# Optimization experiments

Measured on AMD Instinct MI355X. Metric: run time of the kernel, lower is better.

## Reference

```python
import jax, jax.numpy as jnp
import numpy as np

B, S, F, H = 2, 2048, 1024, 16
D = F // H  # 64 head dim


def setup_inputs() -> dict:
    key = jax.random.key(0)
    ks = jax.random.split(key, 11)
    std = 1.0 / np.sqrt(F)
    inp = {
        "q": jax.random.normal(ks[0], (B, S, F), dtype=jnp.float32),
        "k": jax.random.normal(ks[1], (B, S, F), dtype=jnp.float32),
        "v": jax.random.normal(ks[2], (B, S, F), dtype=jnp.float32),
        "wq_w": jax.random.normal(ks[3], (F, F), dtype=jnp.float32) * std,
        "wq_b": jnp.zeros((F,), dtype=jnp.float32),
        "wk_w": jax.random.normal(ks[4], (F, F), dtype=jnp.float32) * std,
        "wk_b": jnp.zeros((F,), dtype=jnp.float32),
        "wv_w": jax.random.normal(ks[5], (F, F), dtype=jnp.float32) * std,
        "wv_b": jnp.zeros((F,), dtype=jnp.float32),
        "fc_w": jax.random.normal(ks[6], (F, F), dtype=jnp.float32) * std,
        "fc_b": jnp.zeros((F,), dtype=jnp.float32),
    }
    return inp


def _split_heads(x):
    # [B, S, F] -> [B, H, S, D]
    return x.reshape(B, S, H, D).transpose(0, 2, 1, 3)


def reference(q, k, v, wq_w, wq_b, wk_w, wk_b, wv_w, wv_b, fc_w, fc_b):
    # Linear projections (torch Linear: x @ W^T + b)
    qh = _split_heads(q @ wq_w.T + wq_b)
    kh = _split_heads(k @ wk_w.T + wk_b)
    vh = _split_heads(v @ wv_w.T + wv_b)
    # scaled dot product attention, explicit [B,H,S,S] scores as in source
    scale = 1.0 / np.sqrt(D)
    scores = jnp.einsum("bhqd,bhkd->bhqk", qh, kh) * scale
    attn = jax.nn.softmax(scores, axis=-1)
    ctx = jnp.einsum("bhqk,bhkd->bhqd", attn, vh)
    # merge heads: [B,H,S,D] -> [B,S,F]
    concat = ctx.transpose(0, 2, 1, 3).reshape(B, S, F)
    out = concat @ fc_w.T + fc_b
    out = jax.nn.relu(out)  # activation=F.relu_ default
    return (out, attn)
```

## Files before the change

### kernel.cpp

```cpp
#include <hip/hip_runtime.h>
#include <stdint.h>

#define DEV __device__ __forceinline__

using f32x4  = __attribute__((ext_vector_type(4))) float;
using bf16x8 = __attribute__((ext_vector_type(8))) __bf16;
using bf16x4 = __attribute__((ext_vector_type(4))) __bf16;

static constexpr int SEQ  = 2048;
static constexpr int FEA  = 1024;
static constexpr int NHEAD = 16;
static constexpr int MROWS = 4096;
static constexpr float QK_SCALE = 0.18033688011112042f;

DEV f32x4 mfma16(bf16x8 a, bf16x8 b, f32x4 c) {
  return __builtin_amdgcn_mfma_f32_16x16x32_bf16(a, b, c, 0, 0, 0);
}

DEV void gload16(const void* g, void* l) {
  __builtin_amdgcn_global_load_lds((__attribute__((address_space(1))) void*)g,
                                   (__attribute__((address_space(3))) void*)l,
                                   16, 0, 0);
}

struct ConvSeg { const float* src; __bf16* dst; int n4; float scale; };
struct ConvArgs { ConvSeg seg[7]; };

__global__ __launch_bounds__(256) void convert_k(ConvArgs a) {
  const ConvSeg sg = a.seg[blockIdx.y];
  const int stride = gridDim.x * blockDim.x;
  for (int i = blockIdx.x * blockDim.x + threadIdx.x; i < sg.n4; i += stride) {
    const f32x4 v = *(const f32x4*)(sg.src + (size_t)i * 4);
    bf16x4 o = {(__bf16)(v[0] * sg.scale), (__bf16)(v[1] * sg.scale),
                (__bf16)(v[2] * sg.scale), (__bf16)(v[3] * sg.scale)};
    *(bf16x4*)(sg.dst + (size_t)i * 4) = o;
  }
}

DEV void gemm_core(const __bf16* __restrict__ A, const __bf16* __restrict__ Bt,
                   char* lds, int row0, int col0, int tid, f32x4 (&acc)[4][4]) {
  char* Alds = lds;
  char* Blds = lds + 8192;
  constexpr int K = 1024;
  const int lane = tid & 63;
  const int w    = tid >> 6;
  const int ci   = lane & 15;
  const int g    = lane >> 4;
  const int wr   = w >> 1, wc = w & 1;

  const int c0 = tid, c1 = tid + 256;
  const __bf16* ga0 = A  + (size_t)(row0 + (c0 >> 2)) * K + (c0 & 3) * 8;
  const __bf16* ga1 = A  + (size_t)(row0 + (c1 >> 2)) * K + (c1 & 3) * 8;
  const __bf16* gb0 = Bt + (size_t)(col0 + (c0 >> 2)) * K + (c0 & 3) * 8;
  const __bf16* gb1 = Bt + (size_t)(col0 + (c1 >> 2)) * K + (c1 & 3) * 8;
  char* la0 = Alds + c0 * 16;
  char* la1 = Alds + c1 * 16;
  char* lb0 = Blds + c0 * 16;
  char* lb1 = Blds + c1 * 16;

  for (int k0 = 0; k0 < K; k0 += 32) {
    __syncthreads();
    gload16(ga0 + k0, la0);
    gload16(ga1 + k0, la1);
    gload16(gb0 + k0, lb0);
    gload16(gb1 + k0, lb1);
    __syncthreads();
    bf16x8 af[4], bfr[4];
#pragma unroll
    for (int m = 0; m < 4; ++m)
      af[m] = *(const bf16x8*)(Alds + ((wr * 64 + m * 16 + ci) * 32 + g * 8) * 2);
#pragma unroll
    for (int n = 0; n < 4; ++n)
      bfr[n] = *(const bf16x8*)(Blds + ((wc * 64 + n * 16 + ci) * 32 + g * 8) * 2);
#pragma unroll
    for (int m = 0; m < 4; ++m)
#pragma unroll
      for (int n = 0; n < 4; ++n)
        acc[m][n] = mfma16(af[m], bfr[n], acc[m][n]);
  }
}

struct QkvArgs {
  const __bf16* A[3];
  const __bf16* Bt[3];
  const float*  bias[3];
  float         bscale[3];
  __bf16*       out[3];
};

__global__ __launch_bounds__(256) void gemm_qkv(QkvArgs args) {
  __shared__ __align__(16) char lds[16384];
  const int z = blockIdx.z;
  const int tid = threadIdx.x;
  const int row0 = blockIdx.x * 128;
  const int col0 = blockIdx.y * 128;
  f32x4 acc[4][4] = {};
  gemm_core(args.A[z], args.Bt[z], lds, row0, col0, tid, acc);

  const int lane = tid & 63;
  const int ci = lane & 15, g = lane >> 4;
  const int w = tid >> 6;
  const int wr = w >> 1, wc = w & 1;
  const float* bias = args.bias[z];
  const float bscale = args.bscale[z];
  __bf16* outp = args.out[z];
  const bool vt = (z == 2);
#pragma unroll
  for (int m = 0; m < 4; ++m)
#pragma unroll
    for (int n = 0; n < 4; ++n)
#pragma unroll
      for (int r = 0; r < 4; ++r) {
        const int gr = row0 + wr * 64 + m * 16 + 4 * g + r;
        const int gc = col0 + wc * 64 + n * 16 + ci;
        const float vv = acc[m][n][r] + bias[gc] * bscale;
        const int b = gr >> 11, s = gr & (SEQ - 1);
        const int h = gc >> 6,  d = gc & 63;
        if (!vt)
          outp[(((size_t)b * NHEAD + h) * SEQ + s) * 64 + d] = (__bf16)vv;
        else
          outp[(((size_t)b * NHEAD + h) * 64 + d) * SEQ + s] = (__bf16)vv;
      }
}

__global__ __launch_bounds__(256) void gemm_fc(const __bf16* __restrict__ A,
                                               const __bf16* __restrict__ Bt,
                                               const float* __restrict__ bias,
                                               float* __restrict__ outp) {
  __shared__ __align__(16) char lds[16384];
  const int tid = threadIdx.x;
  const int row0 = blockIdx.x * 128;
  const int col0 = blockIdx.y * 128;
  f32x4 acc[4][4] = {};
  gemm_core(A, Bt, lds, row0, col0, tid, acc);

  const int lane = tid & 63;
  const int ci = lane & 15, g = lane >> 4;
  const int w = tid >> 6;
  const int wr = w >> 1, wc = w & 1;
#pragma unroll
  for (int m = 0; m < 4; ++m)
#pragma unroll
    for (int n = 0; n < 4; ++n)
#pragma unroll
      for (int r = 0; r < 4; ++r) {
        const int gr = row0 + wr * 64 + m * 16 + 4 * g + r;
        const int gc = col0 + wc * 64 + n * 16 + ci;
        const float vv = fmaxf(acc[m][n][r] + bias[gc], 0.0f);
        __builtin_nontemporal_store(vv, &outp[(size_t)gr * FEA + gc]);
      }
}

static constexpr int QBLK = 32;
static constexpr int KVB  = 128;
static constexpr int NT   = SEQ / KVB;

__global__ __launch_bounds__(512, 8) void attn_fused(const __bf16* __restrict__ Qh,
                                                     const __bf16* __restrict__ Kh,
                                                     const __bf16* __restrict__ VhT,
                                                     float* __restrict__ attn_out,
                                                     __bf16* __restrict__ Cbuf) {
  __shared__ __align__(16) char smem[34816];
  __shared__ float rs_lds[8][16];
  __shared__ float linv_lds[QBLK];
  char* Klds  = smem;
  char* VTlds = smem + 16384;
  float* pvf  = (float*)smem;

  const int tid  = threadIdx.x;
  const int lane = tid & 63;
  const int w    = tid >> 6;
  const int ci   = lane & 15;
  const int g    = lane >> 4;
  const int qg   = w >> 2;
  const int kg   = w & 3;

  const int id   = blockIdx.x;
  const int xcd  = id & 7;
  const int idx  = id >> 3;
  const int bh   = xcd * 4 + (idx >> 6);
  const int qblk = idx & 63;

  const __bf16* Qp   = Qh + ((size_t)bh * SEQ + qblk * QBLK) * 64;
  const char*   Kbyt = (const char*)(Kh  + (size_t)bh * SEQ * 64);
  const char*   Vbyt = (const char*)(VhT + (size_t)bh * 64 * SEQ);

  const int cA = tid, cB = tid + 512;
  const int kswA = (cA * 16) ^ (((cA >> 3) & 7) << 4);
  const int kswB = (cB * 16) ^ (((cB >> 3) & 7) << 4);
  const int vdA = cA >> 4, vdB = cB >> 4;
  const int vswA = vdA * (SEQ * 2) + ((((cA & 15) ^ (vdA & 7))) << 4);
  const int vswB = vdB * (SEQ * 2) + ((((cB & 15) ^ (vdB & 7))) << 4);
  char* kldsA = Klds + cA * 16;
  char* kldsB = Klds + cB * 16;
  char* vldsA = VTlds + cA * 16;
  char* vldsB = VTlds + cB * 16;

  const bf16x8 q0 = *(const bf16x8*)(Qp + (qg * 16 + ci) * 64 + 8 * g);
  const bf16x8 q1 = *(const bf16x8*)(Qp + (qg * 16 + ci) * 64 + 32 + 8 * g);

  const int kswz  = (ci & 7) << 4;
  const int krow0 = kg * 4096 + ci * 128;

  float rs = 0.f;
  for (int t = 0; t < NT; t += 2) {
    __syncthreads();
    gload16(Kbyt + (size_t)t * 16384 + kswA, kldsA);
    gload16(Kbyt + (size_t)t * 16384 + kswB, kldsB);
    gload16(Kbyt + (size_t)(t + 1) * 16384 + kswA, vldsA);
    gload16(Kbyt + (size_t)(t + 1) * 16384 + kswB, vldsB);
    __syncthreads();
#pragma unroll
    for (int hb = 0; hb < 2; ++hb) {
      const char* kt = smem + hb * 16384 + krow0;
#pragma unroll
      for (int s = 0; s < 2; ++s) {
        const bf16x8 k0 = *(const bf16x8*)(kt + s * 2048 + ((16 * g) ^ kswz));
        const bf16x8 k1 = *(const bf16x8*)(kt + s * 2048 + ((64 + 16 * g) ^ kswz));
        f32x4 sf = {0.f, 0.f, 0.f, 0.f};
        sf = mfma16(k0, q0, sf);
        sf = mfma16(k1, q1, sf);
#pragma unroll
        for (int r = 0; r < 4; ++r) rs += __builtin_amdgcn_exp2f(sf[r]);
      }
    }
  }
  rs += __shfl_xor(rs, 16);
  rs += __shfl_xor(rs, 32);
  if (lane < 16) rs_lds[w][lane] = rs;
  __syncthreads();
  if (tid < QBLK) {
    const int qg2 = tid >> 4;
    float tsum = 0.f;
#pragma unroll
    for (int kk = 0; kk < 4; ++kk) tsum += rs_lds[qg2 * 4 + kk][tid & 15];
    linv_lds[tid] = -__log2f(tsum);
  }
  __syncthreads();
  const float linv = linv_lds[qg * 16 + ci];

  f32x4 apv[4] = {};
  float* orow = attn_out + ((size_t)bh * SEQ + qblk * QBLK + qg * 16 + ci) * SEQ +
                kg * 32 + 4 * g;

  for (int t = 0; t < NT; ++t) {
    __syncthreads();
    gload16(Kbyt + (size_t)t * 16384 + kswA, kldsA);
    gload16(Kbyt + (size_t)t * 16384 + kswB, kldsB);
    gload16(Vbyt + (size_t)t * 256 + vswA, vldsA);
    gload16(Vbyt + (size_t)t * 256 + vswB, vldsB);
    __syncthreads();

    f32x4 e[2];
#pragma unroll
    for (int s = 0; s < 2; ++s) {
      const char* kt = Klds + krow0 + s * 2048;
      const bf16x8 k0 = *(const bf16x8*)(kt + ((16 * g) ^ kswz));
      const bf16x8 k1 = *(const bf16x8*)(kt + ((64 + 16 * g) ^ kswz));
      f32x4 sf = {0.f, 0.f, 0.f, 0.f};
      sf = mfma16(k0, q0, sf);
      sf = mfma16(k1, q1, sf);
#pragma unroll
      for (int r = 0; r < 4; ++r) e[s][r] = __builtin_amdgcn_exp2f(sf[r] + linv);
      __builtin_nontemporal_store(e[s], (f32x4*)(orow + t * 128 + s * 16));
    }
    const bf16x8 pa = {(__bf16)e[0][0], (__bf16)e[0][1], (__bf16)e[0][2], (__bf16)e[0][3],
                       (__bf16)e[1][0], (__bf16)e[1][1], (__bf16)e[1][2], (__bf16)e[1][3]};
    const int inr0 = (64 * kg + 8 * g) ^ kswz;
    const int inr1 = (64 * kg + 32 + 8 * g) ^ kswz;
#pragma unroll
    for (int dt = 0; dt < 4; ++dt) {
      const char* vrow = VTlds + (dt * 16 + ci) * 256;
      const bf16x4 v0 = *(const bf16x4*)(vrow + inr0);
      const bf16x4 v1 = *(const bf16x4*)(vrow + inr1);
      const bf16x8 vb = {v0[0], v0[1], v0[2], v0[3], v1[0], v1[1], v1[2], v1[3]};
      apv[dt] = mfma16(pa, vb, apv[dt]);
    }
  }

  __syncthreads();
  {
    const int base = (qg * 4 + kg) * 16;
#pragma unroll
    for (int dt = 0; dt < 4; ++dt)
#pragma unroll
      for (int r = 0; r < 4; ++r)
        pvf[(base + 4 * g + r) * 68 + dt * 16 + ci] = apv[dt][r];
  }
  __syncthreads();
  {
    const int qq  = tid >> 4;
    const int d0  = (tid & 15) * 4;
    const int qg2 = qq >> 4, row = qq & 15;
    f32x4 s = {0.f, 0.f, 0.f, 0.f};
#pragma unroll
    for (int kk = 0; kk < 4; ++kk)
      s += *(const f32x4*)&pvf[((qg2 * 4 + kk) * 16 + row) * 68 + d0];
    const int b = bh >> 4, h = bh & 15;
    const bf16x4 o = {(__bf16)s[0], (__bf16)s[1], (__bf16)s[2], (__bf16)s[3]};
    *(bf16x4*)&Cbuf[((size_t)b * SEQ + qblk * QBLK + qq) * FEA + h * 64 + d0] = o;
  }
}

extern "C" void kernel_launch(void* const* d_in, const int* in_sizes, int n_in,
                              void* d_out, int out_size, void* d_ws, size_t ws_size,
                              hipStream_t stream) {
  const float* q    = (const float*)d_in[0];
  const float* k    = (const float*)d_in[1];
  const float* v    = (const float*)d_in[2];
  const float* wq_w = (const float*)d_in[3];
  const float* wq_b = (const float*)d_in[4];
  const float* wk_w = (const float*)d_in[5];
  const float* wk_b = (const float*)d_in[6];
  const float* wv_w = (const float*)d_in[7];
  const float* wv_b = (const float*)d_in[8];
  const float* fc_w = (const float*)d_in[9];
  const float* fc_b = (const float*)d_in[10];

  float* out0 = (float*)d_out;
  float* attn = out0 + (size_t)MROWS * FEA;

  __bf16* Xq = (__bf16*)attn;
  __bf16* Xk = Xq + (size_t)MROWS * FEA;
  __bf16* Xv = Xk + (size_t)MROWS * FEA;
  __bf16* Wq = Xv + (size_t)MROWS * FEA;
  __bf16* Wk = Wq + (size_t)FEA * FEA;
  __bf16* Wv = Wk + (size_t)FEA * FEA;

  __bf16* Qh  = (__bf16*)d_ws;
  __bf16* Kh  = Qh  + (size_t)MROWS * FEA;
  __bf16* VhT = Kh  + (size_t)MROWS * FEA;
  __bf16* Cb  = VhT + (size_t)MROWS * FEA;
  __bf16* Wfc = Cb  + (size_t)MROWS * FEA;

  ConvArgs ca;
  ca.seg[0] = {q,    Xq,  (MROWS * FEA) / 4, 1.0f};
  ca.seg[1] = {k,    Xk,  (MROWS * FEA) / 4, 1.0f};
  ca.seg[2] = {v,    Xv,  (MROWS * FEA) / 4, 1.0f};
  ca.seg[3] = {wq_w, Wq,  (FEA * FEA) / 4,   QK_SCALE};
  ca.seg[4] = {wk_w, Wk,  (FEA * FEA) / 4,   1.0f};
  ca.seg[5] = {wv_w, Wv,  (FEA * FEA) / 4,   1.0f};
  ca.seg[6] = {fc_w, Wfc, (FEA * FEA) / 4,   1.0f};
  convert_k<<<dim3(512, 7), 256, 0, stream>>>(ca);

  QkvArgs qa;
  qa.A[0] = Xq; qa.Bt[0] = Wq; qa.bias[0] = wq_b; qa.bscale[0] = QK_SCALE; qa.out[0] = Qh;
  qa.A[1] = Xk; qa.Bt[1] = Wk; qa.bias[1] = wk_b; qa.bscale[1] = 1.0f;     qa.out[1] = Kh;
  qa.A[2] = Xv; qa.Bt[2] = Wv; qa.bias[2] = wv_b; qa.bscale[2] = 1.0f;     qa.out[2] = VhT;
  gemm_qkv<<<dim3(MROWS / 128, FEA / 128, 3), 256, 0, stream>>>(qa);

  attn_fused<<<dim3((SEQ / QBLK) * NHEAD * 2), 512, 0, stream>>>(Qh, Kh, VhT, attn, Cb);

  gemm_fc<<<dim3(MROWS / 128, FEA / 128), 256, 0, stream>>>(Cb, Wfc, fc_b, out0);
}
```

Before: 239.3 us.

## Double-buffer K/V tiles in attention and deepen GEMM K-step with swizzled LDS

The attention kernel now prefetches the next K (and V) tile into a second LDS buffer while computing on the current one. It uses explicit vmcnt waits and raw barriers in place of full syncthreads, which targets the load latency that was exposed between tiles. The GEMM core moves from a K-step of 32 to 64 with an XOR-swizzled LDS layout, halving the number of barrier rounds and cutting bank conflicts. LDS use doubles, and attention occupancy is lowered to 4 blocks. The correctness of the vmcnt counts depends on the exact number of outstanding loads.

```diff
diff --git a/kernel.cpp b/kernel.cpp
--- a/kernel.cpp
+++ b/kernel.cpp
@@ -22,6 +22,9 @@
                                    (__attribute__((address_space(3))) void*)l,
                                    16, 0, 0);
 }
+
+#define FENCE_VMCNT(n) asm volatile("s_waitcnt vmcnt(" #n ")" ::: "memory")
+#define FENCE_LGKM0()  asm volatile("s_waitcnt lgkmcnt(0)" ::: "memory")
 
 struct ConvSeg { const float* src; __bf16* dst; int n4; float scale; };
 struct ConvArgs { ConvSeg seg[7]; };
@@ -37,10 +40,10 @@
   }
 }
 
-DEV void gemm_core(const __bf16* __restrict__ A, const __bf16* __restrict__ Bt,
-                   char* lds, int row0, int col0, int tid, f32x4 (&acc)[4][4]) {
+DEV void gemm_core64(const __bf16* __restrict__ A, const __bf16* __restrict__ Bt,
+                     char* lds, int row0, int col0, int tid, f32x4 (&acc)[4][4]) {
   char* Alds = lds;
-  char* Blds = lds + 8192;
+  char* Blds = lds + 16384;
   constexpr int K = 1024;
   const int lane = tid & 63;
   const int w    = tid >> 6;
@@ -48,35 +51,45 @@
   const int g    = lane >> 4;
   const int wr   = w >> 1, wc = w & 1;
 
-  const int c0 = tid, c1 = tid + 256;
-  const __bf16* ga0 = A  + (size_t)(row0 + (c0 >> 2)) * K + (c0 & 3) * 8;
-  const __bf16* ga1 = A  + (size_t)(row0 + (c1 >> 2)) * K + (c1 & 3) * 8;
-  const __bf16* gb0 = Bt + (size_t)(col0 + (c0 >> 2)) * K + (c0 & 3) * 8;
-  const __bf16* gb1 = Bt + (size_t)(col0 + (c1 >> 2)) * K + (c1 & 3) * 8;
-  char* la0 = Alds + c0 * 16;
-  char* la1 = Alds + c1 * 16;
-  char* lb0 = Blds + c0 * 16;
-  char* lb1 = Blds + c1 * 16;
-
-  for (int k0 = 0; k0 < K; k0 += 32) {
+  const __bf16* gA[4]; const __bf16* gB[4];
+  char* lA[4]; char* lB[4];
+#pragma unroll
+  for (int j = 0; j < 4; ++j) {
+    const int c = tid + 256 * j;
+    const int r = c >> 3, s = c & 7;
+    const int gsw = (s ^ (r & 7)) * 8;
+    gA[j] = A  + (size_t)(row0 + r) * K + gsw;
+    gB[j] = Bt + (size_t)(col0 + r) * K + gsw;
+    lA[j] = Alds + c * 16;
+    lB[j] = Blds + c * 16;
+  }
+  const int rsw = (ci & 7) << 4;
+
+  for (int k0 = 0; k0 < K; k0 += 64) {
     __syncthreads();
-    gload16(ga0 + k0, la0);
-    gload16(ga1 + k0, la1);
-    gload16(gb0 + k0, lb0);
-    gload16(gb1 + k0, lb1);
+#pragma unroll
+    for (int j = 0; j < 4; ++j) {
+      gload16(gA[j] + k0, lA[j]);
+      gload16(gB[j] + k0, lB[j]);
+    }
     __syncthreads();
-    bf16x8 af[4], bfr[4];
-#pragma unroll
-    for (int m = 0; m < 4; ++m)
-      af[m] = *(const bf16x8*)(Alds + ((wr * 64 + m * 16 + ci) * 32 + g * 8) * 2);
-#pragma unroll
-    for (int n = 0; n < 4; ++n)
-      bfr[n] = *(const bf16x8*)(Blds + ((wc * 64 + n * 16 + ci) * 32 + g * 8) * 2);
-#pragma unroll
-    for (int m = 0; m < 4; ++m)
+#pragma unroll
+    for (int kk = 0; kk < 2; ++kk) {
+      bf16x8 af[4], bfr[4];
+#pragma unroll
+      for (int m = 0; m < 4; ++m)
+        af[m] = *(const bf16x8*)(Alds + (wr * 64 + m * 16 + ci) * 128 +
+                                 ((kk * 64 + g * 16) ^ rsw));
 #pragma unroll
       for (int n = 0; n < 4; ++n)
-        acc[m][n] = mfma16(af[m], bfr[n], acc[m][n]);
+        bfr[n] = *(const bf16x8*)(Blds + (wc * 64 + n * 16 + ci) * 128 +
+                                  ((kk * 64 + g * 16) ^ rsw));
+#pragma unroll
+      for (int m = 0; m < 4; ++m)
+#pragma unroll
+        for (int n = 0; n < 4; ++n)
+          acc[m][n] = mfma16(af[m], bfr[n], acc[m][n]);
+    }
   }
 }
 
@@ -89,13 +102,13 @@
 };
 
 __global__ __launch_bounds__(256) void gemm_qkv(QkvArgs args) {
-  __shared__ __align__(16) char lds[16384];
+  __shared__ __align__(16) char lds[32768];
   const int z = blockIdx.z;
   const int tid = threadIdx.x;
   const int row0 = blockIdx.x * 128;
   const int col0 = blockIdx.y * 128;
   f32x4 acc[4][4] = {};
-  gemm_core(args.A[z], args.Bt[z], lds, row0, col0, tid, acc);
+  gemm_core64(args.A[z], args.Bt[z], lds, row0, col0, tid, acc);
 
   const int lane = tid & 63;
   const int ci = lane & 15, g = lane >> 4;
@@ -127,12 +140,12 @@
                                                const __bf16* __restrict__ Bt,
                                                const float* __restrict__ bias,
                                                float* __restrict__ outp) {
-  __shared__ __align__(16) char lds[16384];
+  __shared__ __align__(16) char lds[32768];
   const int tid = threadIdx.x;
   const int row0 = blockIdx.x * 128;
   const int col0 = blockIdx.y * 128;
   f32x4 acc[4][4] = {};
-  gemm_core(A, Bt, lds, row0, col0, tid, acc);
+  gemm_core64(A, Bt, lds, row0, col0, tid, acc);
 
   const int lane = tid & 63;
   const int ci = lane & 15, g = lane >> 4;
@@ -155,17 +168,15 @@
 static constexpr int KVB  = 128;
 static constexpr int NT   = SEQ / KVB;
 
-__global__ __launch_bounds__(512, 8) void attn_fused(const __bf16* __restrict__ Qh,
+__global__ __launch_bounds__(512, 4) void attn_fused(const __bf16* __restrict__ Qh,
                                                      const __bf16* __restrict__ Kh,
                                                      const __bf16* __restrict__ VhT,
                                                      float* __restrict__ attn_out,
                                                      __bf16* __restrict__ Cbuf) {
-  __shared__ __align__(16) char smem[34816];
+  __shared__ __align__(16) char smem[65536];
   __shared__ float rs_lds[8][16];
   __shared__ float linv_lds[QBLK];
-  char* Klds  = smem;
-  char* VTlds = smem + 16384;
-  float* pvf  = (float*)smem;
+  float* pvf = (float*)smem;
 
   const int tid  = threadIdx.x;
   const int lane = tid & 63;
@@ -186,15 +197,16 @@
   const char*   Vbyt = (const char*)(VhT + (size_t)bh * 64 * SEQ);
 
   const int cA = tid, cB = tid + 512;
-  const int kswA = (cA * 16) ^ (((cA >> 3) & 7) << 4);
-  const int kswB = (cB * 16) ^ (((cB >> 3) & 7) << 4);
+  const int kgoffA = ((cA >> 3) * 128) + (((cA & 7) ^ ((cA >> 3) & 7)) * 16);
+  const int kgoffB = ((cB >> 3) * 128) + (((cB & 7) ^ ((cB >> 3) & 7)) * 16);
   const int vdA = cA >> 4, vdB = cB >> 4;
-  const int vswA = vdA * (SEQ * 2) + ((((cA & 15) ^ (vdA & 7))) << 4);
-  const int vswB = vdB * (SEQ * 2) + ((((cB & 15) ^ (vdB & 7))) << 4);
-  char* kldsA = Klds + cA * 16;
-  char* kldsB = Klds + cB * 16;
-  char* vldsA = VTlds + cA * 16;
-  char* vldsB = VTlds + cB * 16;
+  const int vgoffA = vdA * (SEQ * 2) + (((cA & 15) ^ (vdA & 7)) * 16);
+  const int vgoffB = vdB * (SEQ * 2) + (((cB & 15) ^ (vdB & 7)) * 16);
+
+#define STAGE_K(t, boff) { gload16(Kbyt + (size_t)(t) * 16384 + kgoffA, smem + (boff) + cA * 16); \
+                           gload16(Kbyt + (size_t)(t) * 16384 + kgoffB, smem + (boff) + cB * 16); }
+#define STAGE_V(t, boff) { gload16(Vbyt + (size_t)(t) * 256 + vgoffA, smem + 16384 + (boff) + cA * 16); \
+                           gload16(Vbyt + (size_t)(t) * 256 + vgoffB, smem + 16384 + (boff) + cB * 16); }
 
   const bf16x8 q0 = *(const bf16x8*)(Qp + (qg * 16 + ci) * 64 + 8 * g);
   const bf16x8 q1 = *(const bf16x8*)(Qp + (qg * 16 + ci) * 64 + 32 + 8 * g);
@@ -203,27 +215,25 @@
   const int krow0 = kg * 4096 + ci * 128;
 
   float rs = 0.f;
-  for (int t = 0; t < NT; t += 2) {
-    __syncthreads();
-    gload16(Kbyt + (size_t)t * 16384 + kswA, kldsA);
-    gload16(Kbyt + (size_t)t * 16384 + kswB, kldsB);
-    gload16(Kbyt + (size_t)(t + 1) * 16384 + kswA, vldsA);
-    gload16(Kbyt + (size_t)(t + 1) * 16384 + kswB, vldsB);
-    __syncthreads();
-#pragma unroll
-    for (int hb = 0; hb < 2; ++hb) {
-      const char* kt = smem + hb * 16384 + krow0;
-#pragma unroll
-      for (int s = 0; s < 2; ++s) {
-        const bf16x8 k0 = *(const bf16x8*)(kt + s * 2048 + ((16 * g) ^ kswz));
-        const bf16x8 k1 = *(const bf16x8*)(kt + s * 2048 + ((64 + 16 * g) ^ kswz));
-        f32x4 sf = {0.f, 0.f, 0.f, 0.f};
-        sf = mfma16(k0, q0, sf);
-        sf = mfma16(k1, q1, sf);
-#pragma unroll
-        for (int r = 0; r < 4; ++r) rs += __builtin_amdgcn_exp2f(sf[r]);
-      }
-    }
+  STAGE_K(0, 0);
+  for (int t = 0; t < NT; ++t) {
+    const int coff = (t & 1) << 15;
+    if (t < NT - 1) { STAGE_K(t + 1, coff ^ 32768); FENCE_VMCNT(2); }
+    else            { FENCE_VMCNT(0); }
+    __builtin_amdgcn_s_barrier();
+    const char* kt = smem + coff + krow0;
+#pragma unroll
+    for (int s = 0; s < 2; ++s) {
+      const bf16x8 k0 = *(const bf16x8*)(kt + s * 2048 + ((16 * g) ^ kswz));
+      const bf16x8 k1 = *(const bf16x8*)(kt + s * 2048 + ((64 + 16 * g) ^ kswz));
+      f32x4 sf = {0.f, 0.f, 0.f, 0.f};
+      sf = mfma16(k0, q0, sf);
+      sf = mfma16(k1, q1, sf);
+#pragma unroll
+      for (int r = 0; r < 4; ++r) rs += __builtin_amdgcn_exp2f(sf[r]);
+    }
+    FENCE_LGKM0();
+    __builtin_amdgcn_s_barrier();
   }
   rs += __shfl_xor(rs, 16);
   rs += __shfl_xor(rs, 32);
@@ -243,18 +253,18 @@
   float* orow = attn_out + ((size_t)bh * SEQ + qblk * QBLK + qg * 16 + ci) * SEQ +
                 kg * 32 + 4 * g;
 
+  STAGE_K(0, 0);
+  STAGE_V(0, 0);
   for (int t = 0; t < NT; ++t) {
-    __syncthreads();
-    gload16(Kbyt + (size_t)t * 16384 + kswA, kldsA);
-    gload16(Kbyt + (size_t)t * 16384 + kswB, kldsB);
-    gload16(Vbyt + (size_t)t * 256 + vswA, vldsA);
-    gload16(Vbyt + (size_t)t * 256 + vswB, vldsB);
-    __syncthreads();
+    const int coff = (t & 1) << 15;
+    if (t < NT - 1) { STAGE_K(t + 1, coff ^ 32768); STAGE_V(t + 1, coff ^ 32768); FENCE_VMCNT(4); }
+    else            { FENCE_VMCNT(0); }
+    __builtin_amdgcn_s_barrier();
 
     f32x4 e[2];
 #pragma unroll
     for (int s = 0; s < 2; ++s) {
-      const char* kt = Klds + krow0 + s * 2048;
+      const char* kt = smem + coff + krow0 + s * 2048;
       const bf16x8 k0 = *(const bf16x8*)(kt + ((16 * g) ^ kswz));
       const bf16x8 k1 = *(const bf16x8*)(kt + ((64 + 16 * g) ^ kswz));
       f32x4 sf = {0.f, 0.f, 0.f, 0.f};
@@ -270,15 +280,16 @@
     const int inr1 = (64 * kg + 32 + 8 * g) ^ kswz;
 #pragma unroll
     for (int dt = 0; dt < 4; ++dt) {
-      const char* vrow = VTlds + (dt * 16 + ci) * 256;
+      const char* vrow = smem + 16384 + coff + (dt * 16 + ci) * 256;
       const bf16x4 v0 = *(const bf16x4*)(vrow + inr0);
       const bf16x4 v1 = *(const bf16x4*)(vrow + inr1);
       const bf16x8 vb = {v0[0], v0[1], v0[2], v0[3], v1[0], v1[1], v1[2], v1[3]};
       apv[dt] = mfma16(pa, vb, apv[dt]);
     }
-  }
-
-  __syncthreads();
+    FENCE_LGKM0();
+    __builtin_amdgcn_s_barrier();
+  }
+
   {
     const int base = (qg * 4 + kg) * 16;
 #pragma unroll
@@ -300,6 +311,8 @@
     const bf16x4 o = {(__bf16)s[0], (__bf16)s[1], (__bf16)s[2], (__bf16)s[3]};
     *(bf16x4*)&Cbuf[((size_t)b * SEQ + qblk * QBLK + qq) * FEA + h * 64 + d0] = o;
   }
+#undef STAGE_K
+#undef STAGE_V
 }
 
 extern "C" void kernel_launch(void* const* d_in, const int* in_sizes, int n_in,
```

New measurement: 236.1 us. No clear change (-1.3%).
